# Optimization experiments

Measured on AMD Instinct MI355X. Metric: run time of the kernel, lower is better.

The kernel has to match this reference:

```python
import jax, jax.numpy as jnp
import numpy as np

V, E_DIM, HID, GNN_O, HEADS = 50257, 256, 128, 128, 4
N_NODES, N_EDGES, T_LEN = 10000, 160000, 64
NEG_SLOPE = 0.2


def gatv2(x, src, dst, Wl, Wr, att, bias, concat):
    """PyG GATv2Conv (share_weights=False, self-loops already in src/dst)."""
    heads, out_ch = att.shape
    n = x.shape[0]
    xl = (x @ Wl).reshape(n, heads, out_ch)   # source transform
    xr = (x @ Wr).reshape(n, heads, out_ch)   # target transform
    e = jax.nn.leaky_relu(xl[src] + xr[dst], NEG_SLOPE)        # [E, h, c]
    logits = jnp.einsum('ehc,hc->eh', e, att)                  # [E, h]
    m = jax.ops.segment_max(logits, dst, num_segments=n)
    a = jnp.exp(logits - m[dst])
    a = a / jax.ops.segment_sum(a, dst, num_segments=n)[dst]
    out = jax.ops.segment_sum(xl[src] * a[..., None], dst, num_segments=n)
    out = out.reshape(n, heads * out_ch) if concat else out.mean(axis=1)
    return out + bias


def setup_inputs() -> dict:
    key = jax.random.key(0)
    ks = jax.random.split(key, 16)
    g = lambda k, shape: jax.random.normal(k, shape, jnp.float32) * 0.05
    x_nodes = jax.random.randint(ks[0], (N_NODES,), 0, V)
    edge_index = jax.random.randint(ks[1], (2, N_EDGES), 0, N_NODES)
    target_sequence = jax.random.randint(ks[2], (1, T_LEN), 0, V)
    return dict(
        x_nodes=x_nodes, edge_index=edge_index, target_sequence=target_sequence,
        embedding=g(ks[3], (V, E_DIM)),
        W1l=g(ks[4], (E_DIM, HEADS * HID)), W1r=g(ks[5], (E_DIM, HEADS * HID)),
        att1=g(ks[6], (HEADS, HID)), b1=jnp.zeros((HEADS * HID,), jnp.float32),
        W2l=g(ks[7], (HEADS * HID, GNN_O)), W2r=g(ks[8], (HEADS * HID, GNN_O)),
        att2=g(ks[9], (1, GNN_O)), b2=jnp.zeros((GNN_O,), jnp.float32),
        Wih=g(ks[10], (3 * HID, GNN_O + E_DIM)), Whh=g(ks[11], (3 * HID, HID)),
        bih=jnp.zeros((3 * HID,), jnp.float32), bhh=jnp.zeros((3 * HID,), jnp.float32),
        Wout=g(ks[12], (V, HID)), bout=jnp.zeros((V,), jnp.float32),
    )


def reference(x_nodes, edge_index, target_sequence, embedding,
              W1l, W1r, att1, b1, W2l, W2r, att2, b2,
              Wih, Whh, bih, bhh, Wout, bout):
    n = x_nodes.shape[0]
    loops = jnp.arange(n, dtype=edge_index.dtype)
    src = jnp.concatenate([edge_index[0], loops])   # add self-loops (PyG default)
    dst = jnp.concatenate([edge_index[1], loops])
    feats = embedding[x_nodes]                      # [N, E_DIM] (dropout off: eval)
    h1 = jax.nn.elu(gatv2(feats, src, dst, W1l, W1r, att1, b1, concat=True))
    enc = gatv2(h1, src, dst, W2l, W2r, att2, b2, concat=False)  # [N, GNN_O]
    context = enc.mean(axis=0)                      # constant across decode steps

    # teacher forcing (ratio=1.0): input tokens are SOS(0) then shifted targets
    tokens = jnp.concatenate([jnp.zeros((1,), target_sequence.dtype),
                              target_sequence[0, :-1]])

    def step(h, tok):
        x = jnp.concatenate([embedding[tok], context])          # [E_DIM+GNN_O]
        gi = Wih @ x + bih
        gh = Whh @ h + bhh
        ir, iz, inn = jnp.split(gi, 3)
        hr, hz, hn = jnp.split(gh, 3)
        r = jax.nn.sigmoid(ir + hr)
        z = jax.nn.sigmoid(iz + hz)
        cand = jnp.tanh(inn + r * hn)
        h_new = (1.0 - z) * cand + z * h
        logits = Wout @ h_new + bout
        return h_new, logits

    h0 = jnp.zeros((Whh.shape[1],), jnp.float32)
    _, logits = jax.lax.scan(step, h0, tokens)      # [T, V]
    return logits[None]                              # [1, T, V]
```

## Files before the change

kernel.cpp:

```cpp
#include <hip/hip_runtime.h>
#include <hip/hip_bf16.h>
#include <math.h>

#define NNODES 10000
#define NEDGES 160000
#define EDIM   256
#define HIDC   128
#define TLEN   64
#define VOCAB  50257
#define NEG    0.2f
#define NCTXSLOT 32

typedef __bf16 bf16x8 __attribute__((ext_vector_type(8)));
typedef float  f32x4  __attribute__((ext_vector_type(4)));

static __device__ __forceinline__ float leaky(float x){ return x > 0.f ? x : NEG*x; }
static __device__ __forceinline__ float sigm (float x){ return __fdividef(1.f, 1.f + __expf(-x)); }
static __device__ __forceinline__ float eluf (float x){ return x > 0.f ? x : expm1f(x); }
static __device__ __forceinline__ unsigned short bf16rn(float f){
  unsigned a = __float_as_uint(f);
  return (unsigned short)((a + 0x7FFFu + ((a >> 16) & 1u)) >> 16);
}
static __device__ __forceinline__ float upf(unsigned short u){ return __uint_as_float(((unsigned)u) << 16); }

#define PB_FEATS 2500
#define PB_WCAST 8783
#define PB_TR1L  8815
#define PB_TR1R  8847
#define PB_TR2L  8863
#define PB_TR2R  8879
#define PB_ZERO  8919
#define PB_AT    9047

static __device__ void tr_dev(const float* __restrict__ in, unsigned short* __restrict__ out,
                              int K, int Nin, int bx, int by, int t,
                              unsigned short (*tile)[72])
{
  int k0 = bx*64, n0 = by*64;
  int tr = t >> 4, tc4 = (t & 15)*4;
  #pragma unroll
  for (int it = 0; it < 4; ++it){
    int kr = tr + 16*it;
    float4 v = *(const float4*)(in + (size_t)(k0+kr)*Nin + n0 + tc4);
    tile[tc4+0][kr] = bf16rn(v.x);
    tile[tc4+1][kr] = bf16rn(v.y);
    tile[tc4+2][kr] = bf16rn(v.z);
    tile[tc4+3][kr] = bf16rn(v.w);
  }
  __syncthreads();
  #pragma unroll
  for (int it = 0; it < 4; ++it){
    int nr = tr + 16*it;
    ushort4 o;
    o.x = tile[nr][tc4+0]; o.y = tile[nr][tc4+1];
    o.z = tile[nr][tc4+2]; o.w = tile[nr][tc4+3];
    *(ushort4*)(out + (size_t)(n0+nr)*K + k0 + tc4) = o;
  }
}

__global__ __launch_bounds__(256) void k_prep(
    const int* __restrict__ xn, const float* __restrict__ emb,
    unsigned short* __restrict__ featsb,
    const float* __restrict__ Wout, unsigned short* __restrict__ Woutb,
    const float* __restrict__ W1l, const float* __restrict__ W1r, unsigned short* __restrict__ Bt1,
    const float* __restrict__ W2l, const float* __restrict__ W2r, unsigned short* __restrict__ Bt2,
    int* __restrict__ deg, int* __restrict__ cursor, float* __restrict__ ctxp,
    const int* __restrict__ tseq, const float* __restrict__ Wih,
    const float* __restrict__ bih, float* __restrict__ At)
{
  __shared__ unsigned short tile[64][72];
  __shared__ __align__(16) float xe[EDIM];
  int b = blockIdx.x, t = threadIdx.x;
  if (b < PB_FEATS){
    int node = b*4 + (t >> 6);
    int l = t & 63;
    float4 v = ((const float4*)(emb + (size_t)xn[node]*EDIM))[l];
    ushort4 o; o.x = bf16rn(v.x); o.y = bf16rn(v.y); o.z = bf16rn(v.z); o.w = bf16rn(v.w);
    *(ushort4*)(featsb + (size_t)node*EDIM + 4*l) = o;
  } else if (b < PB_WCAST){
    int idx = (b - PB_FEATS)*256 + t;
    if (idx < VOCAB*HIDC/4){
      float4 v = ((const float4*)Wout)[idx];
      ushort4 o; o.x = bf16rn(v.x); o.y = bf16rn(v.y); o.z = bf16rn(v.z); o.w = bf16rn(v.w);
      ((ushort4*)Woutb)[idx] = o;
    }
  } else if (b < PB_TR1L){
    int lb = b - PB_WCAST;  tr_dev(W1l, Bt1,           256, 512, lb & 3, lb >> 2, t, tile);
  } else if (b < PB_TR1R){
    int lb = b - PB_TR1L;   tr_dev(W1r, Bt1 + 512*256, 256, 512, lb & 3, lb >> 2, t, tile);
  } else if (b < PB_TR2L){
    int lb = b - PB_TR1R;   tr_dev(W2l, Bt2,           512, 128, lb & 7, lb >> 3, t, tile);
  } else if (b < PB_TR2R){
    int lb = b - PB_TR2L;   tr_dev(W2r, Bt2 + 128*512, 512, 128, lb & 7, lb >> 3, t, tile);
  } else if (b < PB_ZERO){
    int gid = (b - PB_TR2R)*256 + t;
    if (gid < NNODES){ deg[gid] = 0; cursor[gid] = 0; }
    if (gid < NCTXSLOT*HIDC) ctxp[gid] = 0.f;
  } else {
    int lb = b - PB_ZERO;
    int tt = lb >> 1;
    int row = (lb & 1)*192 + t;
    int tok = (tt == 0) ? 0 : tseq[tt-1];
    {
      if (t < 64) ((float4*)xe)[t] = ((const float4*)(emb + (size_t)tok*EDIM))[t];
      __syncthreads();
    }
    if (t < 192){
      const float4* w4 = (const float4*)(Wih + (size_t)row*384);
      const float4* x4 = (const float4*)xe;
      float a0 = 0.f, a1 = 0.f, a2 = 0.f, a3 = 0.f;
      #pragma unroll
      for (int k = 0; k < 64; k++){
        float4 w = w4[k]; float4 x = x4[k];
        a0 = fmaf(w.x, x.x, a0); a1 = fmaf(w.y, x.y, a1);
        a2 = fmaf(w.z, x.z, a2); a3 = fmaf(w.w, x.w, a3);
      }
      At[tt*384 + row] = ((a0 + a1) + (a2 + a3)) + bih[row];
    }
  }
}

__global__ void k_deg(const int* __restrict__ dst, int* __restrict__ deg){
  int e = blockIdx.x*256 + threadIdx.x;
  if (e < NEDGES) atomicAdd(&deg[dst[e]], 1);
}

__global__ __launch_bounds__(1024) void k_scan(const int* __restrict__ deg, int* __restrict__ offs){
  __shared__ int s[1024];
  int t = threadIdx.x;
  int loc[10]; int sum = 0;
  #pragma unroll
  for (int q = 0; q < 10; q++){
    int idx = t*10 + q;
    loc[q] = sum;
    sum += (idx < NNODES) ? deg[idx] : 0;
  }
  s[t] = sum;
  __syncthreads();
  for (int ofs = 1; ofs < 1024; ofs <<= 1){
    int v = (t >= ofs) ? s[t-ofs] : 0;
    __syncthreads();
    s[t] += v;
    __syncthreads();
  }
  int pre = (t > 0) ? s[t-1] : 0;
  #pragma unroll
  for (int q = 0; q < 10; q++){
    int idx = t*10 + q;
    if (idx < NNODES) offs[idx] = pre + loc[q];
  }
  if (t == 1023) offs[NNODES] = s[1023];
}

__global__ void k_scatter(const int* __restrict__ src, const int* __restrict__ dst,
                          const int* __restrict__ offs, int* __restrict__ cursor,
                          int* __restrict__ esrc){
  int e = blockIdx.x*256 + threadIdx.x;
  if (e >= NEDGES) return;
  int d = dst[e];
  int p = atomicAdd(&cursor[d], 1);
  esrc[offs[d] + p] = src[e];
}

template<int KDIM>
__global__ __launch_bounds__(256) void k_mfma(const unsigned short* __restrict__ A,
    const unsigned short* __restrict__ Bt, unsigned short* __restrict__ C,
    int M, int N)
{
  __shared__ __align__(16) unsigned short As[128*64];
  __shared__ __align__(16) unsigned short Bs[128*64];
  int tid = threadIdx.x;
  int l   = tid & 63;
  int wid = tid >> 6;
  int wr = wid >> 1, wc = wid & 1;
  int row0 = blockIdx.x * 128, col0 = blockIdx.y * 128;
  int lr = l & 15, kg = l >> 4;
  f32x4 acc[4][4] = {};

  for (int kt = 0; kt < KDIM/64; ++kt){
    int k0 = kt*64;
    #pragma unroll
    for (int c = 0; c < 4; ++c){
      int chunk = wid*4 + c;
      int arow = row0 + chunk*8 + (l >> 3);
      if (arow > M-1) arow = M-1;
      const unsigned short* ga = A + (size_t)arow*KDIM + k0 + (l & 7)*8;
      __builtin_amdgcn_global_load_lds(
          (const __attribute__((address_space(1))) void*)ga,
          (__attribute__((address_space(3))) void*)(As + chunk*512), 16, 0, 0);
      int brow = col0 + chunk*8 + (l >> 3);
      const unsigned short* gb = Bt + (size_t)brow*KDIM + k0 + (l & 7)*8;
      __builtin_amdgcn_global_load_lds(
          (const __attribute__((address_space(1))) void*)gb,
          (__attribute__((address_space(3))) void*)(Bs + chunk*512), 16, 0, 0);
    }
    __syncthreads();
    #pragma unroll
    for (int ks = 0; ks < 2; ++ks){
      bf16x8 af[4], bfr[4];
      #pragma unroll
      for (int m = 0; m < 4; ++m)
        af[m] = *(const bf16x8*)(As + (wr*64 + m*16 + lr)*64 + ks*32 + kg*8);
      #pragma unroll
      for (int n = 0; n < 4; ++n)
        bfr[n] = *(const bf16x8*)(Bs + (wc*64 + n*16 + lr)*64 + ks*32 + kg*8);
      #pragma unroll
      for (int m = 0; m < 4; ++m)
        #pragma unroll
        for (int n = 0; n < 4; ++n)
          acc[m][n] = __builtin_amdgcn_mfma_f32_16x16x32_bf16(af[m], bfr[n], acc[m][n], 0, 0, 0);
    }
    __syncthreads();
  }

  #pragma unroll
  for (int m = 0; m < 4; ++m){
    int rbase = row0 + wr*64 + m*16 + kg*4;
    #pragma unroll
    for (int r = 0; r < 4; ++r){
      int row = rbase + r;
      if (row < M){
        #pragma unroll
        for (int n = 0; n < 4; ++n){
          int col = col0 + wc*64 + n*16 + lr;
          C[(size_t)row*N + col] = bf16rn(acc[m][n][r]);
        }
      }
    }
  }
}

__global__ __launch_bounds__(256) void k_mout(const unsigned short* __restrict__ A,
    const unsigned short* __restrict__ Bt, const float* __restrict__ bias,
    float* __restrict__ out)
{
  __shared__ __align__(16) unsigned short As[64*128];
  __shared__ __align__(16) unsigned short Bs[128*128];
  int tid = threadIdx.x;
  int l   = tid & 63;
  int wid = tid >> 6;
  int col0 = blockIdx.x * 128;
  int lr = l & 15, kg = l >> 4;

  #pragma unroll
  for (int c = 0; c < 4; ++c){
    int chunk = wid*4 + c;
    const unsigned short* ga = A + (size_t)(chunk*4 + (l >> 4))*128 + (l & 15)*8;
    __builtin_amdgcn_global_load_lds(
        (const __attribute__((address_space(1))) void*)ga,
        (__attribute__((address_space(3))) void*)(As + chunk*512), 16, 0, 0);
  }
  #pragma unroll
  for (int c = 0; c < 8; ++c){
    int chunk = wid*8 + c;
    int brow = col0 + chunk*4 + (l >> 4);
    if (brow > VOCAB-1) brow = VOCAB-1;
    const unsigned short* gb = Bt + (size_t)brow*128 + (l & 15)*8;
    __builtin_amdgcn_global_load_lds(
        (const __attribute__((address_space(1))) void*)gb,
        (__attribute__((address_space(3))) void*)(Bs + chunk*512), 16, 0, 0);
  }
  __syncthreads();

  f32x4 acc[4][2] = {};
  #pragma unroll
  for (int ks = 0; ks < 4; ++ks){
    bf16x8 af[4], bfr[2];
    #pragma unroll
    for (int m = 0; m < 4; ++m)
      af[m] = *(const bf16x8*)(As + (m*16 + lr)*128 + ks*32 + kg*8);
    #pragma unroll
    for (int n = 0; n < 2; ++n)
      bfr[n] = *(const bf16x8*)(Bs + (wid*32 + n*16 + lr)*128 + ks*32 + kg*8);
    #pragma unroll
    for (int m = 0; m < 4; ++m)
      #pragma unroll
      for (int n = 0; n < 2; ++n)
        acc[m][n] = __builtin_amdgcn_mfma_f32_16x16x32_bf16(af[m], bfr[n], acc[m][n], 0, 0, 0);
  }

  #pragma unroll
  for (int n = 0; n < 2; ++n){
    int col = col0 + wid*32 + n*16 + lr;
    if (col < VOCAB){
      float bv = bias[col];
      #pragma unroll
      for (int m = 0; m < 4; ++m){
        #pragma unroll
        for (int r = 0; r < 4; ++r){
          int trow = m*16 + kg*4 + r;
          out[(size_t)trow*VOCAB + col] = acc[m][n][r] + bv;
        }
      }
    }
  }
}

__global__ __launch_bounds__(256) void k_gat1(const unsigned short* __restrict__ xlr,
    const int* __restrict__ esrc, const int* __restrict__ offs,
    const float* __restrict__ att, const float* __restrict__ b1,
    unsigned short* __restrict__ h1b)
{
  int node = blockIdx.x*4 + (threadIdx.x >> 6);
  int l = threadIdx.x & 63;
  const unsigned short* bi = xlr + (size_t)node*1024;
  ushort4 u;
  u = *(const ushort4*)(bi + 512 + 4*l);
  float4 xr1; xr1.x = upf(u.x); xr1.y = upf(u.y); xr1.z = upf(u.z); xr1.w = upf(u.w);
  u = *(const ushort4*)(bi + 768 + 4*l);
  float4 xr2; xr2.x = upf(u.x); xr2.y = upf(u.y); xr2.z = upf(u.z); xr2.w = upf(u.w);
  int hq = l >> 5;
  float4 at1 = *(const float4*)(att + hq*HIDC + ((4*l) & 127));
  float4 at2 = *(const float4*)(att + (2+hq)*HIDC + ((4*l) & 127));
  float4 ac1 = {0,0,0,0}, ac2 = {0,0,0,0};
  float d1 = 0.f, d2 = 0.f;
  int beg = offs[node], end = offs[node+1];
  for (int p = beg-1; p < end; ++p){
    int s = (p < beg) ? node : esrc[p];
    const unsigned short* bs = xlr + (size_t)s*1024;
    ushort4 u1 = *(const ushort4*)(bs + 4*l);
    ushort4 u2 = *(const ushort4*)(bs + 256 + 4*l);
    float4 x1; x1.x = upf(u1.x); x1.y = upf(u1.y); x1.z = upf(u1.z); x1.w = upf(u1.w);
    float4 x2; x2.x = upf(u2.x); x2.y = upf(u2.y); x2.z = upf(u2.z); x2.w = upf(u2.w);
    float p1 = leaky(x1.x+xr1.x)*at1.x + leaky(x1.y+xr1.y)*at1.y
             + leaky(x1.z+xr1.z)*at1.z + leaky(x1.w+xr1.w)*at1.w;
    float p2 = leaky(x2.x+xr2.x)*at2.x + leaky(x2.y+xr2.y)*at2.y
             + leaky(x2.z+xr2.z)*at2.z + leaky(x2.w+xr2.w)*at2.w;
    #pragma unroll
    for (int m = 1; m <= 16; m <<= 1){
      p1 += __shfl_xor(p1, m);
      p2 += __shfl_xor(p2, m);
    }
    float w1 = __expf(p1), w2 = __expf(p2);
    ac1.x = fmaf(w1, x1.x, ac1.x); ac1.y = fmaf(w1, x1.y, ac1.y);
    ac1.z = fmaf(w1, x1.z, ac1.z); ac1.w = fmaf(w1, x1.w, ac1.w);
    ac2.x = fmaf(w2, x2.x, ac2.x); ac2.y = fmaf(w2, x2.y, ac2.y);
    ac2.z = fmaf(w2, x2.z, ac2.z); ac2.w = fmaf(w2, x2.w, ac2.w);
    d1 += w1; d2 += w2;
  }
  float i1 = 1.f/d1, i2 = 1.f/d2;
  const float* bq1 = b1 + 4*l;
  const float* bq2 = b1 + 256 + 4*l;
  ushort4 o1, o2;
  o1.x = bf16rn(eluf(ac1.x*i1 + bq1[0])); o1.y = bf16rn(eluf(ac1.y*i1 + bq1[1]));
  o1.z = bf16rn(eluf(ac1.z*i1 + bq1[2])); o1.w = bf16rn(eluf(ac1.w*i1 + bq1[3]));
  o2.x = bf16rn(eluf(ac2.x*i2 + bq2[0])); o2.y = bf16rn(eluf(ac2.y*i2 + bq2[1]));
  o2.z = bf16rn(eluf(ac2.z*i2 + bq2[2])); o2.w = bf16rn(eluf(ac2.w*i2 + bq2[3]));
  *(ushort4*)(h1b + (size_t)node*512 + 4*l)       = o1;
  *(ushort4*)(h1b + (size_t)node*512 + 256 + 4*l) = o2;
}

__global__ __launch_bounds__(256) void k_gat2(const unsigned short* __restrict__ xlr2,
    const int* __restrict__ esrc, const int* __restrict__ offs,
    const float* __restrict__ att2, float* __restrict__ ctxp)
{
  __shared__ float csum[128];
  int node = blockIdx.x*4 + (threadIdx.x >> 6);
  int l = threadIdx.x & 63;
  if (threadIdx.x < 128) csum[threadIdx.x] = 0.f;
  __syncthreads();
  const unsigned short* bi = xlr2 + (size_t)node*256;
  ushort2 v = *(const ushort2*)(bi + 128 + 2*l);
  float2 xr; xr.x = upf(v.x); xr.y = upf(v.y);
  float2 at = *(const float2*)(att2 + 2*l);
  float2 ac = {0,0}; float den = 0.f;
  int beg = offs[node], end = offs[node+1];
  for (int p = beg-1; p < end; ++p){
    int s = (p < beg) ? node : esrc[p];
    ushort2 xv = *(const ushort2*)(xlr2 + (size_t)s*256 + 2*l);
    float2 x; x.x = upf(xv.x); x.y = upf(xv.y);
    float pp = leaky(x.x+xr.x)*at.x + leaky(x.y+xr.y)*at.y;
    #pragma unroll
    for (int m = 1; m <= 32; m <<= 1) pp += __shfl_xor(pp, m);
    float w = __expf(pp);
    ac.x = fmaf(w, x.x, ac.x); ac.y = fmaf(w, x.y, ac.y);
    den += w;
  }
  float inv = 1.f/den;
  atomicAdd(&csum[2*l],   ac.x*inv);
  atomicAdd(&csum[2*l+1], ac.y*inv);
  __syncthreads();
  if (threadIdx.x < 128)
    atomicAdd(&ctxp[(blockIdx.x & (NCTXSLOT-1))*HIDC + threadIdx.x],
              csum[threadIdx.x] * (1.f/NNODES));
}

__global__ __launch_bounds__(384) void k_ctx(const float* __restrict__ At,
    const float* __restrict__ ctxp, const float* __restrict__ b2,
    const float* __restrict__ Wih, float* __restrict__ Gi)
{
  __shared__ alignas(16) float CTX[128];
  int tid = threadIdx.x;
  if (tid < 128){
    float s = 0.f;
    #pragma unroll
    for (int j = 0; j < NCTXSLOT; ++j) s += ctxp[j*HIDC + tid];
    CTX[tid] = s + b2[tid];
  }
  __syncthreads();
  const float4* wi = (const float4*)(Wih + (size_t)tid*384 + 256);
  const float4* c4 = (const float4*)CTX;
  float a0 = 0.f, a1 = 0.f, a2 = 0.f, a3 = 0.f;
  #pragma unroll
  for (int k = 0; k < 32; k++){
    float4 ww = wi[k]; float4 cc = c4[k];
    a0 = fmaf(ww.x, cc.x, a0); a1 = fmaf(ww.y, cc.y, a1);
    a2 = fmaf(ww.z, cc.z, a2); a3 = fmaf(ww.w, cc.w, a3);
  }
  float c = ((a0 + a1) + (a2 + a3));
  for (int t = 0; t < TLEN; t++)
    Gi[t*384 + tid] = At[t*384 + tid] + c;
}

__global__ __launch_bounds__(384) void k_gru(const float* __restrict__ Gi,
    const float* __restrict__ Whh, const float* __restrict__ bhh,
    unsigned short* __restrict__ HTt)
{
  __shared__ float GH[384];
  __shared__ alignas(16) float HS[128];
  int tid = threadIdx.x;
  float w[128];
  {
    const float4* wrow = (const float4*)(Whh + (size_t)tid*HIDC);
    #pragma unroll
    for (int k = 0; k < 32; k++){
      float4 v = wrow[k];
      w[4*k+0] = v.x; w[4*k+1] = v.y; w[4*k+2] = v.z; w[4*k+3] = v.w;
    }
  }
  float bh = bhh[tid];
  float hloc = 0.f;
  if (tid < 128) HS[tid] = 0.f;
  __syncthreads();

  const float4* H4 = (const float4*)HS;

  for (int t = 0; t < TLEN; t++){
    float gi0 = 0.f, gi1 = 0.f, gi2 = 0.f;
    if (tid < 128){
      gi0 = Gi[t*384 + tid];
      gi1 = Gi[t*384 + 128 + tid];
      gi2 = Gi[t*384 + 256 + tid];
    }
    float a0 = 0.f, a1 = 0.f, a2 = 0.f, a3 = 0.f;
    #pragma unroll
    for (int q = 0; q < 16; q++){
      float4 ha = H4[2*q];
      float4 hb = H4[2*q+1];
      a0 = fmaf(w[8*q+0], ha.x, a0);
      a1 = fmaf(w[8*q+1], ha.y, a1);
      a2 = fmaf(w[8*q+2], ha.z, a2);
      a3 = fmaf(w[8*q+3], ha.w, a3);
      a0 = fmaf(w[8*q+4], hb.x, a0);
      a1 = fmaf(w[8*q+5], hb.y, a1);
      a2 = fmaf(w[8*q+6], hb.z, a2);
      a3 = fmaf(w[8*q+7], hb.w, a3);
    }
    float acc = ((a0 + a1) + (a2 + a3)) + bh;
    if (tid >= 128) GH[tid] = acc;
    __syncthreads();
    if (tid < 128){
      float gr = gi0 + acc;
      float gz = gi1 + GH[128 + tid];
      float hn = GH[256 + tid];
      float r = sigm(gr);
      float z = sigm(gz);
      float e2 = __expf(2.f*(gi2 + r*hn));
      float cand = __fdividef(e2 - 1.f, e2 + 1.f);
      float hnew = (1.f - z)*cand + z*hloc;
      hloc = hnew;
      HS[tid] = hnew;
      HTt[t*HIDC + tid] = bf16rn(hnew);
    }
    __syncthreads();
  }
}

extern "C" void kernel_launch(void* const* d_in, const int* in_sizes, int n_in,
                              void* d_out, int out_size, void* d_ws, size_t ws_size,
                              hipStream_t stream)
{
  const int*   x_nodes = (const int*)  d_in[0];
  const int*   eidx    = (const int*)  d_in[1];
  const int*   tseq    = (const int*)  d_in[2];
  const float* emb     = (const float*)d_in[3];
  const float* W1l     = (const float*)d_in[4];
  const float* W1r     = (const float*)d_in[5];
  const float* att1    = (const float*)d_in[6];
  const float* b1      = (const float*)d_in[7];
  const float* W2l     = (const float*)d_in[8];
  const float* W2r     = (const float*)d_in[9];
  const float* att2    = (const float*)d_in[10];
  const float* b2      = (const float*)d_in[11];
  const float* Wih     = (const float*)d_in[12];
  const float* Whh     = (const float*)d_in[13];
  const float* bih     = (const float*)d_in[14];
  const float* bhh     = (const float*)d_in[15];
  const float* Wout    = (const float*)d_in[16];
  const float* bout    = (const float*)d_in[17];
  float* out = (float*)d_out;
  char*  ws  = (char*)d_ws;

  unsigned short* xlr1b  = (unsigned short*)(ws);
  unsigned short* h1b    = (unsigned short*)(ws + 20480000);
  unsigned short* featsb = (unsigned short*)(ws + 30720000);
  unsigned short* xlr2b  = (unsigned short*)(ws + 35840000);
  unsigned short* Bt1    = (unsigned short*)(ws + 46080000);
  unsigned short* Bt2    = (unsigned short*)(ws + 46604288);
  int*   deg    = (int*)(ws + 46866432);
  int*   offs   = (int*)(ws + 46906432);
  int*   cursor = (int*)(ws + 46946436);
  int*   esrc   = (int*)(ws + 46986436);
  float* At     = (float*)(ws + 47627008);
  unsigned short* HTt   = (unsigned short*)(ws + 47725312);
  unsigned short* Woutb = (unsigned short*)(ws + 47741696);
  float* ctxp   = (float*)(ws + 60607488);
  float* Gi     = (float*)(ws + 60623872);

  k_prep<<<PB_AT, 256, 0, stream>>>(x_nodes, emb, featsb, Wout, Woutb,
                                    W1l, W1r, Bt1, W2l, W2r, Bt2,
                                    deg, cursor, ctxp, tseq, Wih, bih, At);

  k_deg    <<<625, 256, 0, stream>>>(eidx + NEDGES, deg);
  k_scan   <<<1,  1024, 0, stream>>>(deg, offs);
  k_scatter<<<625, 256, 0, stream>>>(eidx, eidx + NEDGES, offs, cursor, esrc);

  k_mfma<256><<<dim3(79,8), 256, 0, stream>>>(featsb, Bt1, xlr1b, NNODES, 1024);
  k_gat1<<<2500, 256, 0, stream>>>(xlr1b, esrc, offs, att1, b1, h1b);

  k_mfma<512><<<dim3(79,2), 256, 0, stream>>>(h1b, Bt2, xlr2b, NNODES, 256);
  k_gat2<<<2500, 256, 0, stream>>>(xlr2b, esrc, offs, att2, ctxp);

  k_ctx<<<1, 384, 0, stream>>>(At, ctxp, b2, Wih, Gi);
  k_gru<<<1, 384, 0, stream>>>(Gi, Whh, bhh, HTt);

  k_mout<<<393, 256, 0, stream>>>(HTt, Woutb, bout, out);
}
```

Baseline: 250.7 us.

## Split xl/xr GEMM outputs into separate buffers and prefetch gathered rows in GAT loops

The MFMA GEMM now writes the source-transform and target-transform halves into two separate contiguous arrays. Gathered source rows then sit densely packed, 1 KB per node instead of strided across 2 KB rows, which should improve cache-line and L2 locality for the random gather. Both GAT aggregation loops are software-pipelined: the next neighbour's row and the index two edges ahead are loaded before computing on the current row, hiding dependent-load latency. This adds registers and an extra speculative load per node.

```diff
diff --git a/kernel.cpp b/kernel.cpp
--- a/kernel.cpp
+++ b/kernel.cpp
@@ -22,6 +22,9 @@
   return (unsigned short)((a + 0x7FFFu + ((a >> 16) & 1u)) >> 16);
 }
 static __device__ __forceinline__ float upf(unsigned short u){ return __uint_as_float(((unsigned)u) << 16); }
+static __device__ __forceinline__ float4 up4(ushort4 u){
+  float4 f; f.x = upf(u.x); f.y = upf(u.y); f.z = upf(u.z); f.w = upf(u.w); return f;
+}
 
 #define PB_FEATS 2500
 #define PB_WCAST 8783
@@ -164,7 +167,8 @@
 
 template<int KDIM>
 __global__ __launch_bounds__(256) void k_mfma(const unsigned short* __restrict__ A,
-    const unsigned short* __restrict__ Bt, unsigned short* __restrict__ C,
+    const unsigned short* __restrict__ Bt,
+    unsigned short* __restrict__ C0, unsigned short* __restrict__ C1,
     int M, int N)
 {
   __shared__ __align__(16) unsigned short As[128*64];
@@ -213,6 +217,9 @@
     __syncthreads();
   }
 
+  int half = N >> 1;
+  unsigned short* Cp = (col0 < half) ? C0 : C1;
+  int cb = (col0 < half) ? col0 : col0 - half;
   #pragma unroll
   for (int m = 0; m < 4; ++m){
     int rbase = row0 + wr*64 + m*16 + kg*4;
@@ -222,8 +229,8 @@
       if (row < M){
         #pragma unroll
         for (int n = 0; n < 4; ++n){
-          int col = col0 + wc*64 + n*16 + lr;
-          C[(size_t)row*N + col] = bf16rn(acc[m][n][r]);
+          int col = cb + wc*64 + n*16 + lr;
+          Cp[(size_t)row*half + col] = bf16rn(acc[m][n][r]);
         }
       }
     }
@@ -296,32 +303,34 @@
   }
 }
 
-__global__ __launch_bounds__(256) void k_gat1(const unsigned short* __restrict__ xlr,
+__global__ __launch_bounds__(256) void k_gat1(const unsigned short* __restrict__ xl,
+    const unsigned short* __restrict__ xr,
     const int* __restrict__ esrc, const int* __restrict__ offs,
     const float* __restrict__ att, const float* __restrict__ b1,
     unsigned short* __restrict__ h1b)
 {
   int node = blockIdx.x*4 + (threadIdx.x >> 6);
   int l = threadIdx.x & 63;
-  const unsigned short* bi = xlr + (size_t)node*1024;
-  ushort4 u;
-  u = *(const ushort4*)(bi + 512 + 4*l);
-  float4 xr1; xr1.x = upf(u.x); xr1.y = upf(u.y); xr1.z = upf(u.z); xr1.w = upf(u.w);
-  u = *(const ushort4*)(bi + 768 + 4*l);
-  float4 xr2; xr2.x = upf(u.x); xr2.y = upf(u.y); xr2.z = upf(u.z); xr2.w = upf(u.w);
+  const unsigned short* ri = xr + (size_t)node*512;
+  float4 xr1 = up4(*(const ushort4*)(ri + 4*l));
+  float4 xr2 = up4(*(const ushort4*)(ri + 256 + 4*l));
   int hq = l >> 5;
   float4 at1 = *(const float4*)(att + hq*HIDC + ((4*l) & 127));
   float4 at2 = *(const float4*)(att + (2+hq)*HIDC + ((4*l) & 127));
   float4 ac1 = {0,0,0,0}, ac2 = {0,0,0,0};
   float d1 = 0.f, d2 = 0.f;
   int beg = offs[node], end = offs[node+1];
+  int sB = (beg < end) ? esrc[beg] : 0;
+  const unsigned short* rA = xl + (size_t)node*512;
+  ushort4 uA1 = *(const ushort4*)(rA + 4*l);
+  ushort4 uA2 = *(const ushort4*)(rA + 256 + 4*l);
   for (int p = beg-1; p < end; ++p){
-    int s = (p < beg) ? node : esrc[p];
-    const unsigned short* bs = xlr + (size_t)s*1024;
-    ushort4 u1 = *(const ushort4*)(bs + 4*l);
-    ushort4 u2 = *(const ushort4*)(bs + 256 + 4*l);
-    float4 x1; x1.x = upf(u1.x); x1.y = upf(u1.y); x1.z = upf(u1.z); x1.w = upf(u1.w);
-    float4 x2; x2.x = upf(u2.x); x2.y = upf(u2.y); x2.z = upf(u2.z); x2.w = upf(u2.w);
+    const unsigned short* rB = xl + (size_t)sB*512;
+    ushort4 uB1 = *(const ushort4*)(rB + 4*l);
+    ushort4 uB2 = *(const ushort4*)(rB + 256 + 4*l);
+    int sC = (p+2 < end) ? esrc[p+2] : 0;
+    float4 x1 = up4(uA1);
+    float4 x2 = up4(uA2);
     float p1 = leaky(x1.x+xr1.x)*at1.x + leaky(x1.y+xr1.y)*at1.y
              + leaky(x1.z+xr1.z)*at1.z + leaky(x1.w+xr1.w)*at1.w;
     float p2 = leaky(x2.x+xr2.x)*at2.x + leaky(x2.y+xr2.y)*at2.y
@@ -337,6 +346,7 @@
     ac2.x = fmaf(w2, x2.x, ac2.x); ac2.y = fmaf(w2, x2.y, ac2.y);
     ac2.z = fmaf(w2, x2.z, ac2.z); ac2.w = fmaf(w2, x2.w, ac2.w);
     d1 += w1; d2 += w2;
+    uA1 = uB1; uA2 = uB2; sB = sC;
   }
   float i1 = 1.f/d1, i2 = 1.f/d2;
   const float* bq1 = b1 + 4*l;
@@ -350,7 +360,8 @@
   *(ushort4*)(h1b + (size_t)node*512 + 256 + 4*l) = o2;
 }
 
-__global__ __launch_bounds__(256) void k_gat2(const unsigned short* __restrict__ xlr2,
+__global__ __launch_bounds__(256) void k_gat2(const unsigned short* __restrict__ xl,
+    const unsigned short* __restrict__ xr,
     const int* __restrict__ esrc, const int* __restrict__ offs,
     const float* __restrict__ att2, float* __restrict__ ctxp)
 {
@@ -359,22 +370,24 @@
   int l = threadIdx.x & 63;
   if (threadIdx.x < 128) csum[threadIdx.x] = 0.f;
   __syncthreads();
-  const unsigned short* bi = xlr2 + (size_t)node*256;
-  ushort2 v = *(const ushort2*)(bi + 128 + 2*l);
-  float2 xr; xr.x = upf(v.x); xr.y = upf(v.y);
+  ushort2 v = *(const ushort2*)(xr + (size_t)node*128 + 2*l);
+  float2 xrv; xrv.x = upf(v.x); xrv.y = upf(v.y);
   float2 at = *(const float2*)(att2 + 2*l);
   float2 ac = {0,0}; float den = 0.f;
   int beg = offs[node], end = offs[node+1];
+  int sB = (beg < end) ? esrc[beg] : 0;
+  ushort2 uA = *(const ushort2*)(xl + (size_t)node*128 + 2*l);
   for (int p = beg-1; p < end; ++p){
-    int s = (p < beg) ? node : esrc[p];
-    ushort2 xv = *(const ushort2*)(xlr2 + (size_t)s*256 + 2*l);
-    float2 x; x.x = upf(xv.x); x.y = upf(xv.y);
-    float pp = leaky(x.x+xr.x)*at.x + leaky(x.y+xr.y)*at.y;
+    ushort2 uB = *(const ushort2*)(xl + (size_t)sB*128 + 2*l);
+    int sC = (p+2 < end) ? esrc[p+2] : 0;
+    float2 x; x.x = upf(uA.x); x.y = upf(uA.y);
+    float pp = leaky(x.x+xrv.x)*at.x + leaky(x.y+xrv.y)*at.y;
     #pragma unroll
     for (int m = 1; m <= 32; m <<= 1) pp += __shfl_xor(pp, m);
     float w = __expf(pp);
     ac.x = fmaf(w, x.x, ac.x); ac.y = fmaf(w, x.y, ac.y);
     den += w;
+    uA = uB; sB = sC;
   }
   float inv = 1.f/den;
   atomicAdd(&csum[2*l],   ac.x*inv);
@@ -501,10 +514,12 @@
   float* out = (float*)d_out;
   char*  ws  = (char*)d_ws;
 
-  unsigned short* xlr1b  = (unsigned short*)(ws);
+  unsigned short* xl1b   = (unsigned short*)(ws);
+  unsigned short* xr1b   = (unsigned short*)(ws + 10240000);
   unsigned short* h1b    = (unsigned short*)(ws + 20480000);
   unsigned short* featsb = (unsigned short*)(ws + 30720000);
-  unsigned short* xlr2b  = (unsigned short*)(ws + 35840000);
+  unsigned short* xl2b   = (unsigned short*)(ws + 35840000);
+  unsigned short* xr2b   = (unsigned short*)(ws + 38400000);
   unsigned short* Bt1    = (unsigned short*)(ws + 46080000);
   unsigned short* Bt2    = (unsigned short*)(ws + 46604288);
   int*   deg    = (int*)(ws + 46866432);
@@ -525,11 +540,11 @@
   k_scan   <<<1,  1024, 0, stream>>>(deg, offs);
   k_scatter<<<625, 256, 0, stream>>>(eidx, eidx + NEDGES, offs, cursor, esrc);
 
-  k_mfma<256><<<dim3(79,8), 256, 0, stream>>>(featsb, Bt1, xlr1b, NNODES, 1024);
-  k_gat1<<<2500, 256, 0, stream>>>(xlr1b, esrc, offs, att1, b1, h1b);
-
-  k_mfma<512><<<dim3(79,2), 256, 0, stream>>>(h1b, Bt2, xlr2b, NNODES, 256);
-  k_gat2<<<2500, 256, 0, stream>>>(xlr2b, esrc, offs, att2, ctxp);
+  k_mfma<256><<<dim3(79,8), 256, 0, stream>>>(featsb, Bt1, xl1b, xr1b, NNODES, 1024);
+  k_gat1<<<2500, 256, 0, stream>>>(xl1b, xr1b, esrc, offs, att1, b1, h1b);
+
+  k_mfma<512><<<dim3(79,2), 256, 0, stream>>>(h1b, Bt2, xl2b, xr2b, NNODES, 256);
+  k_gat2<<<2500, 256, 0, stream>>>(xl2b, xr2b, esrc, offs, att2, ctxp);
 
   k_ctx<<<1, 384, 0, stream>>>(At, ctxp, b2, Wih, Gi);
   k_gru<<<1, 384, 0, stream>>>(Gi, Whh, bhh, HTt);
```

Result: faster. 243.0 us (-3.1%).
